# Optimization experiments

Hardware: AMD Instinct MI355X
Metric: run time of the kernel (lower is better)

The kernel has to match this reference:

```python
import jax, jax.numpy as jnp
import numpy as np

M_TOP = 30      # top-M candidates per query
K_NB = 20       # K+1 nearest within candidate set (K=19)
BETA = 0.15


def setup_inputs() -> dict:
    key = jax.random.key(0)
    k1, k2, k3 = jax.random.split(key, 3)
    N, D, B, R = 500000, 512, 4096, 1000
    X = jax.random.normal(k1, (N, D), dtype=jnp.float32)
    Q = jax.random.normal(k2, (B, D), dtype=jnp.float32)
    ranks = jax.random.randint(k3, (R, B), 0, N, dtype=jnp.int64)
    return {"X": X, "Q": Q, "ranks": ranks}


def reference(X, Q, ranks):
    # ranks: [n_ranked, B] -> take top-M candidate ids per query: [B, M]
    rt = ranks.T[:, :M_TOP]                       # [B, M]
    Xt = X[rt]                                    # gather: [B, M, D]
    # batched self-similarity among the M candidates
    sim = jnp.einsum('bmd,bnd->bmn', Xt, Xt)      # [B, M, M]
    # descending sort, keep top K_NB values+indices (== -sort(-sim)[:K], argsort(-sim)[:K])
    vals, idx = jax.lax.top_k(sim, K_NB)          # [B, M, K]
    # weights: first neighbor (self) weight 1.0, rest scaled by beta
    w = jnp.concatenate([jnp.ones_like(vals[..., :1]), vals[..., 1:] * BETA], axis=-1)
    w = w[..., None]                              # [B, M, K, 1]
    # gather neighbor descriptors within each query's candidate set
    # x_g[b,m,k,d] = Xt[b, idx[b,m,k], d]
    x_g = jnp.take_along_axis(Xt[:, None, :, :], idx[..., None], axis=2)  # [B, M, K, D]
    # weighted average over the K neighbors
    x_dba = jnp.sum(x_g * w, axis=2) / jnp.sum(w, axis=2)                 # [B, M, D]
    # rerank candidates against the query descriptor
    scores = jnp.einsum('bd,bmd->bm', Q, x_dba)   # [B, M]
    order = jnp.argsort(-scores, axis=-1)         # [B, M]
    rerank = jnp.take_along_axis(rt, order, axis=1)  # [B, M] final db ids
    return rerank, scores, order, x_dba
```

## Files before the change

### kernel.cpp

```cpp
#include <hip/hip_runtime.h>
#include <stdint.h>

#define MT   30
#define KNB  20
#define DD   512
#define SROW 68
#define MWS  32

#define PR(r) ((((r) & 1) * 15) + ((r) >> 1))

extern "C" __global__ void __launch_bounds__(256, 6)
mdesc_fused(const float* __restrict__ X, const float* __restrict__ Q,
            const int* __restrict__ ranks, float* __restrict__ out, int B)
{
    __shared__ alignas(16) char arrA[MT * SROW * 4];
    __shared__ alignas(16) float QS[DD];
    __shared__ double simS[MT][MT + 1];
    __shared__ double qdotPart[MT][8];
    __shared__ double qdotS[MT];
    __shared__ int    rtS[MT];

    float  (*XtS)[SROW] = (float(*)[SROW])arrA;
    float  (*MwS)[MWS]  = (float(*)[MWS])arrA;
    double *scoreS      = (double*)(arrA + 3840);
    int    *orderS      = (int*)(arrA + 4080);

    const int b = blockIdx.x;
    const int tid = threadIdx.x;

    if (tid < MT) rtS[tid] = ranks[(size_t)tid * B + b];
    __syncthreads();

    const bool isSim = (tid < 120);
    const bool isQ   = (tid >= 128 && tid < 248);
    int i0 = 0, i1 = 0, j0 = 0, j1 = 0;
    if (isSim) {
        int I = 0, rem = tid;
        while (rem >= 15 - I) { rem -= 15 - I; ++I; }
        int J = I + rem;
        i0 = 2 * I; i1 = i0 + 1; j0 = 2 * J; j1 = j0 + 1;
    }
    const int qm = (tid - 128) >> 2;
    const int qs = (tid - 128) & 3;

    double a00 = 0.0, a01 = 0.0, a10 = 0.0, a11 = 0.0;

    for (int st = 0; st < 8; ++st) {
        for (int i = tid; i < MT * 16; i += 256) {
            int row = i >> 4;
            int k = i & 15;
            float4 v = *(const float4*)(X + (size_t)rtS[row] * DD + st * 64 + (k << 2));
            *(float4*)(&XtS[PR(row)][k << 2]) = v;
        }
        if (st == 0 && tid < 128) {
            float4 v = *(const float4*)(Q + (size_t)b * DD + (tid << 2));
            *(float4*)(&QS[tid << 2]) = v;
        }
        __syncthreads();

        if (isSim) {
            const float* R0 = &XtS[PR(i0)][0];
            const float* R1 = &XtS[PR(i1)][0];
            const float* C0 = &XtS[PR(j0)][0];
            const float* C1 = &XtS[PR(j1)][0];
            for (int k = 0; k < 16; ++k) {
                float4 va0 = *(const float4*)(R0 + (k << 2));
                float4 va1 = *(const float4*)(R1 + (k << 2));
                float4 vb0 = *(const float4*)(C0 + (k << 2));
                float4 vb1 = *(const float4*)(C1 + (k << 2));
                const float* A0 = (const float*)&va0;
                const float* A1 = (const float*)&va1;
                const float* B0 = (const float*)&vb0;
                const float* B1 = (const float*)&vb1;
                #pragma unroll
                for (int c = 0; c < 4; ++c) {
                    double x0 = (double)A0[c], x1 = (double)A1[c];
                    double y0 = (double)B0[c], y1 = (double)B1[c];
                    a00 = fma(x0, y0, a00);
                    a01 = fma(x0, y1, a01);
                    a10 = fma(x1, y0, a10);
                    a11 = fma(x1, y1, a11);
                }
            }
            if (st == 3) {
                simS[i0][j0] = a00; simS[i0][j1] = a01;
                simS[i1][j0] = a10; simS[i1][j1] = a11;
                a00 = a01 = a10 = a11 = 0.0;
            }
            if (st == 7) {
                double s00 = simS[i0][j0] + a00;
                double s01 = simS[i0][j1] + a01;
                double s10 = simS[i1][j0] + a10;
                double s11 = simS[i1][j1] + a11;
                simS[i0][j0] = s00; simS[j0][i0] = s00;
                simS[i0][j1] = s01; simS[j1][i0] = s01;
                simS[i1][j0] = s10; simS[j0][i1] = s10;
                simS[i1][j1] = s11; simS[j1][i1] = s11;
            }
        }
        if (isQ && (st & 3) == qs) {
            double acc = 0.0;
            const float* xr = &XtS[PR(qm)][0];
            for (int k = 0; k < 16; ++k) {
                float4 q4 = *(const float4*)(&QS[(st * 16 + k) << 2]);
                float4 x4 = *(const float4*)(xr + (k << 2));
                const float* qq = (const float*)&q4;
                const float* xx = (const float*)&x4;
                #pragma unroll
                for (int c = 0; c < 4; ++c)
                    acc = fma((double)qq[c], (double)xx[c], acc);
            }
            qdotPart[qm][st] = acc;
        }
        __syncthreads();
    }

    for (int i = tid; i < MT * MWS; i += 256) (&MwS[0][0])[i] = 0.0f;
    __syncthreads();

    const size_t sec = (size_t)B * MT;
    if (tid < MT) {
        {
            double acc = 0.0;
            #pragma unroll
            for (int s = 0; s < 8; ++s) acc += qdotPart[tid][s];
            qdotS[tid] = acc;
        }
        const int m = tid;
        unsigned used = 0;
        double Wsum = 0.0, sAcc = 0.0;
        for (int k = 0; k < KNB; ++k) {
            double best = -1.0e300; int bj = 0;
            for (int j = 0; j < MT; ++j) {
                if (used & (1u << j)) continue;
                double v = simS[m][j];
                if (v > best) { best = v; bj = j; }
            }
            used |= (1u << bj);
            double w = (k == 0) ? 1.0 : best * 0.15;
            Wsum += w;
            sAcc = fma(w, qdotS[bj], sAcc);
            MwS[m][bj] = (float)w;
        }
        scoreS[m] = sAcc / Wsum;
        float inv = (float)(1.0 / Wsum);
        for (int j = 0; j < MT; ++j)
            if (used & (1u << j)) MwS[m][j] *= inv;
        double mysc = scoreS[tid];
        int pos = 0;
        for (int j = 0; j < MT; ++j) {
            double v = scoreS[j];
            if (v > mysc || (v == mysc && j < tid)) ++pos;
        }
        orderS[pos] = tid;
        int r = tid;
        int src = orderS[r];
        out[(size_t)b * MT + r]            = (float)rtS[src];
        out[sec + (size_t)b * MT + tid]    = (float)scoreS[tid];
        out[2 * sec + (size_t)b * MT + r]  = (float)src;
    }
    __syncthreads();

    {
        const int sub = tid >> 7;
        const int c   = tid & 127;
        const int r0  = sub * 15;
        float4 acc[15];
        #pragma unroll
        for (int r = 0; r < 15; ++r) acc[r] = make_float4(0.f, 0.f, 0.f, 0.f);

        for (int jg = 0; jg < 15; ++jg) {
            const int ja = 2 * jg, jb = ja + 1;
            float4 xv0 = *(const float4*)(X + (size_t)rtS[ja] * DD + (c << 2));
            float4 xv1 = *(const float4*)(X + (size_t)rtS[jb] * DD + (c << 2));
            #pragma unroll
            for (int r = 0; r < 15; ++r) {
                float2 wv = *(const float2*)&MwS[r0 + r][ja];
                acc[r].x = fmaf(wv.x, xv0.x, acc[r].x);
                acc[r].x = fmaf(wv.y, xv1.x, acc[r].x);
                acc[r].y = fmaf(wv.x, xv0.y, acc[r].y);
                acc[r].y = fmaf(wv.y, xv1.y, acc[r].y);
                acc[r].z = fmaf(wv.x, xv0.z, acc[r].z);
                acc[r].z = fmaf(wv.y, xv1.z, acc[r].z);
                acc[r].w = fmaf(wv.x, xv0.w, acc[r].w);
                acc[r].w = fmaf(wv.y, xv1.w, acc[r].w);
            }
        }

        const size_t xbase = 3 * sec;
        #pragma unroll
        for (int r = 0; r < 15; ++r) {
            *(float4*)(out + xbase + ((size_t)b * MT + (r0 + r)) * DD + (c << 2)) = acc[r];
        }
    }
}

extern "C" void kernel_launch(void* const* d_in, const int* in_sizes, int n_in,
                              void* d_out, int out_size, void* d_ws, size_t ws_size,
                              hipStream_t stream)
{
    const float* X = (const float*)d_in[0];
    const float* Q = (const float*)d_in[1];
    const int* ranks = (const int*)d_in[2];
    const int B = in_sizes[1] / DD;
    mdesc_fused<<<dim3(B), dim3(256), 0, stream>>>(X, Q, ranks, (float*)d_out, B);
}
```

Baseline: 248.6 us.

## Halve block size and use 3x3 register tiles for similarity

Blocks shrink from 256 to 128 threads. The similarity upper triangle is now covered by 55 threads, each computing a 3x3 double tile, instead of 120 threads each doing a 2x2 tile. Each of 30 threads computes its full query dot product, replacing the four-way split. The weighted-average phase loops twice over 15-row groups per thread. This aims to cut idle threads and raise reuse per shared load, but gives less parallelism per block, slower FP64 chains per thread, and drops the padded row permutation that avoided bank conflicts.

```diff
diff --git a/kernel.cpp b/kernel.cpp
--- a/kernel.cpp
+++ b/kernel.cpp
@@ -7,9 +7,7 @@
 #define SROW 68
 #define MWS  32
 
-#define PR(r) ((((r) & 1) * 15) + ((r) >> 1))
-
-extern "C" __global__ void __launch_bounds__(256, 6)
+extern "C" __global__ void __launch_bounds__(128, 4)
 mdesc_fused(const float* __restrict__ X, const float* __restrict__ Q,
             const int* __restrict__ ranks, float* __restrict__ out, int B)
 {
@@ -31,76 +29,89 @@
     if (tid < MT) rtS[tid] = ranks[(size_t)tid * B + b];
     __syncthreads();
 
-    const bool isSim = (tid < 120);
-    const bool isQ   = (tid >= 128 && tid < 248);
-    int i0 = 0, i1 = 0, j0 = 0, j1 = 0;
+    const bool isSim = (tid < 55);
+    int i0 = 0, j0 = 0;
     if (isSim) {
         int I = 0, rem = tid;
-        while (rem >= 15 - I) { rem -= 15 - I; ++I; }
-        int J = I + rem;
-        i0 = 2 * I; i1 = i0 + 1; j0 = 2 * J; j1 = j0 + 1;
-    }
-    const int qm = (tid - 128) >> 2;
-    const int qs = (tid - 128) & 3;
-
-    double a00 = 0.0, a01 = 0.0, a10 = 0.0, a11 = 0.0;
+        while (rem >= 10 - I) { rem -= 10 - I; ++I; }
+        i0 = 3 * I; j0 = 3 * (I + rem);
+    }
+    const bool isQ = (tid >= 64 && tid < 64 + MT);
+    const int qm = tid - 64;
+
+    double a00 = 0.0, a01 = 0.0, a02 = 0.0;
+    double a10 = 0.0, a11 = 0.0, a12 = 0.0;
+    double a20 = 0.0, a21 = 0.0, a22 = 0.0;
 
     for (int st = 0; st < 8; ++st) {
-        for (int i = tid; i < MT * 16; i += 256) {
+        for (int i = tid; i < MT * 16; i += 128) {
             int row = i >> 4;
             int k = i & 15;
             float4 v = *(const float4*)(X + (size_t)rtS[row] * DD + st * 64 + (k << 2));
-            *(float4*)(&XtS[PR(row)][k << 2]) = v;
-        }
-        if (st == 0 && tid < 128) {
+            *(float4*)(&XtS[row][k << 2]) = v;
+        }
+        if (st == 0) {
             float4 v = *(const float4*)(Q + (size_t)b * DD + (tid << 2));
             *(float4*)(&QS[tid << 2]) = v;
         }
         __syncthreads();
 
         if (isSim) {
-            const float* R0 = &XtS[PR(i0)][0];
-            const float* R1 = &XtS[PR(i1)][0];
-            const float* C0 = &XtS[PR(j0)][0];
-            const float* C1 = &XtS[PR(j1)][0];
+            const float* R0 = &XtS[i0][0];
+            const float* R1 = &XtS[i0 + 1][0];
+            const float* R2 = &XtS[i0 + 2][0];
+            const float* C0 = &XtS[j0][0];
+            const float* C1 = &XtS[j0 + 1][0];
+            const float* C2 = &XtS[j0 + 2][0];
             for (int k = 0; k < 16; ++k) {
                 float4 va0 = *(const float4*)(R0 + (k << 2));
                 float4 va1 = *(const float4*)(R1 + (k << 2));
+                float4 va2 = *(const float4*)(R2 + (k << 2));
                 float4 vb0 = *(const float4*)(C0 + (k << 2));
                 float4 vb1 = *(const float4*)(C1 + (k << 2));
+                float4 vb2 = *(const float4*)(C2 + (k << 2));
                 const float* A0 = (const float*)&va0;
                 const float* A1 = (const float*)&va1;
+                const float* A2 = (const float*)&va2;
                 const float* B0 = (const float*)&vb0;
                 const float* B1 = (const float*)&vb1;
+                const float* B2 = (const float*)&vb2;
                 #pragma unroll
                 for (int c = 0; c < 4; ++c) {
-                    double x0 = (double)A0[c], x1 = (double)A1[c];
-                    double y0 = (double)B0[c], y1 = (double)B1[c];
-                    a00 = fma(x0, y0, a00);
-                    a01 = fma(x0, y1, a01);
-                    a10 = fma(x1, y0, a10);
-                    a11 = fma(x1, y1, a11);
+                    double x0 = (double)A0[c], x1 = (double)A1[c], x2 = (double)A2[c];
+                    double y0 = (double)B0[c], y1 = (double)B1[c], y2 = (double)B2[c];
+                    a00 = fma(x0, y0, a00); a01 = fma(x0, y1, a01); a02 = fma(x0, y2, a02);
+                    a10 = fma(x1, y0, a10); a11 = fma(x1, y1, a11); a12 = fma(x1, y2, a12);
+                    a20 = fma(x2, y0, a20); a21 = fma(x2, y1, a21); a22 = fma(x2, y2, a22);
                 }
             }
             if (st == 3) {
-                simS[i0][j0] = a00; simS[i0][j1] = a01;
-                simS[i1][j0] = a10; simS[i1][j1] = a11;
-                a00 = a01 = a10 = a11 = 0.0;
+                simS[i0    ][j0] = a00; simS[i0    ][j0 + 1] = a01; simS[i0    ][j0 + 2] = a02;
+                simS[i0 + 1][j0] = a10; simS[i0 + 1][j0 + 1] = a11; simS[i0 + 1][j0 + 2] = a12;
+                simS[i0 + 2][j0] = a20; simS[i0 + 2][j0 + 1] = a21; simS[i0 + 2][j0 + 2] = a22;
+                a00 = a01 = a02 = a10 = a11 = a12 = a20 = a21 = a22 = 0.0;
             }
             if (st == 7) {
-                double s00 = simS[i0][j0] + a00;
-                double s01 = simS[i0][j1] + a01;
-                double s10 = simS[i1][j0] + a10;
-                double s11 = simS[i1][j1] + a11;
-                simS[i0][j0] = s00; simS[j0][i0] = s00;
-                simS[i0][j1] = s01; simS[j1][i0] = s01;
-                simS[i1][j0] = s10; simS[j0][i1] = s10;
-                simS[i1][j1] = s11; simS[j1][i1] = s11;
-            }
-        }
-        if (isQ && (st & 3) == qs) {
+                double h00v = simS[i0    ][j0]; double h01v = simS[i0    ][j0 + 1]; double h02v = simS[i0    ][j0 + 2];
+                double h10v = simS[i0 + 1][j0]; double h11v = simS[i0 + 1][j0 + 1]; double h12v = simS[i0 + 1][j0 + 2];
+                double h20v = simS[i0 + 2][j0]; double h21v = simS[i0 + 2][j0 + 1]; double h22v = simS[i0 + 2][j0 + 2];
+                double s00 = h00v + a00, s01 = h01v + a01, s02 = h02v + a02;
+                double s10 = h10v + a10, s11 = h11v + a11, s12 = h12v + a12;
+                double s20 = h20v + a20, s21 = h21v + a21, s22 = h22v + a22;
+                simS[i0    ][j0] = s00; simS[j0    ][i0] = s00;
+                simS[i0    ][j0 + 1] = s01; simS[j0 + 1][i0] = s01;
+                simS[i0    ][j0 + 2] = s02; simS[j0 + 2][i0] = s02;
+                simS[i0 + 1][j0] = s10; simS[j0    ][i0 + 1] = s10;
+                simS[i0 + 1][j0 + 1] = s11; simS[j0 + 1][i0 + 1] = s11;
+                simS[i0 + 1][j0 + 2] = s12; simS[j0 + 2][i0 + 1] = s12;
+                simS[i0 + 2][j0] = s20; simS[j0    ][i0 + 2] = s20;
+                simS[i0 + 2][j0 + 1] = s21; simS[j0 + 1][i0 + 2] = s21;
+                simS[i0 + 2][j0 + 2] = s22; simS[j0 + 2][i0 + 2] = s22;
+            }
+        }
+        if (isQ) {
             double acc = 0.0;
-            const float* xr = &XtS[PR(qm)][0];
+            const float* xr = &XtS[qm][0];
             for (int k = 0; k < 16; ++k) {
                 float4 q4 = *(const float4*)(&QS[(st * 16 + k) << 2]);
                 float4 x4 = *(const float4*)(xr + (k << 2));
@@ -115,7 +126,7 @@
         __syncthreads();
     }
 
-    for (int i = tid; i < MT * MWS; i += 256) (&MwS[0][0])[i] = 0.0f;
+    for (int i = tid; i < MT * MWS; i += 128) (&MwS[0][0])[i] = 0.0f;
     __syncthreads();
 
     const size_t sec = (size_t)B * MT;
@@ -162,35 +173,36 @@
     __syncthreads();
 
     {
-        const int sub = tid >> 7;
-        const int c   = tid & 127;
-        const int r0  = sub * 15;
-        float4 acc[15];
+        const int c = tid;
+        const size_t xbase = 3 * sec;
         #pragma unroll
-        for (int r = 0; r < 15; ++r) acc[r] = make_float4(0.f, 0.f, 0.f, 0.f);
-
-        for (int jg = 0; jg < 15; ++jg) {
-            const int ja = 2 * jg, jb = ja + 1;
-            float4 xv0 = *(const float4*)(X + (size_t)rtS[ja] * DD + (c << 2));
-            float4 xv1 = *(const float4*)(X + (size_t)rtS[jb] * DD + (c << 2));
+        for (int g = 0; g < 2; ++g) {
+            const int r0 = g * 15;
+            float4 acc[15];
+            #pragma unroll
+            for (int r = 0; r < 15; ++r) acc[r] = make_float4(0.f, 0.f, 0.f, 0.f);
+
+            for (int jg = 0; jg < 15; ++jg) {
+                const int ja = 2 * jg, jb = ja + 1;
+                float4 xv0 = *(const float4*)(X + (size_t)rtS[ja] * DD + (c << 2));
+                float4 xv1 = *(const float4*)(X + (size_t)rtS[jb] * DD + (c << 2));
+                #pragma unroll
+                for (int r = 0; r < 15; ++r) {
+                    float2 wv = *(const float2*)&MwS[r0 + r][ja];
+                    acc[r].x = fmaf(wv.x, xv0.x, acc[r].x);
+                    acc[r].x = fmaf(wv.y, xv1.x, acc[r].x);
+                    acc[r].y = fmaf(wv.x, xv0.y, acc[r].y);
+                    acc[r].y = fmaf(wv.y, xv1.y, acc[r].y);
+                    acc[r].z = fmaf(wv.x, xv0.z, acc[r].z);
+                    acc[r].z = fmaf(wv.y, xv1.z, acc[r].z);
+                    acc[r].w = fmaf(wv.x, xv0.w, acc[r].w);
+                    acc[r].w = fmaf(wv.y, xv1.w, acc[r].w);
+                }
+            }
             #pragma unroll
             for (int r = 0; r < 15; ++r) {
-                float2 wv = *(const float2*)&MwS[r0 + r][ja];
-                acc[r].x = fmaf(wv.x, xv0.x, acc[r].x);
-                acc[r].x = fmaf(wv.y, xv1.x, acc[r].x);
-                acc[r].y = fmaf(wv.x, xv0.y, acc[r].y);
-                acc[r].y = fmaf(wv.y, xv1.y, acc[r].y);
-                acc[r].z = fmaf(wv.x, xv0.z, acc[r].z);
-                acc[r].z = fmaf(wv.y, xv1.z, acc[r].z);
-                acc[r].w = fmaf(wv.x, xv0.w, acc[r].w);
-                acc[r].w = fmaf(wv.y, xv1.w, acc[r].w);
-            }
-        }
-
-        const size_t xbase = 3 * sec;
-        #pragma unroll
-        for (int r = 0; r < 15; ++r) {
-            *(float4*)(out + xbase + ((size_t)b * MT + (r0 + r)) * DD + (c << 2)) = acc[r];
+                *(float4*)(out + xbase + ((size_t)b * MT + (r0 + r)) * DD + (c << 2)) = acc[r];
+            }
         }
     }
 }
@@ -203,5 +215,5 @@
     const float* Q = (const float*)d_in[1];
     const int* ranks = (const int*)d_in[2];
     const int B = in_sizes[1] / DD;
-    mdesc_fused<<<dim3(B), dim3(256), 0, stream>>>(X, Q, ranks, (float*)d_out, B);
+    mdesc_fused<<<dim3(B), dim3(128), 0, stream>>>(X, Q, ranks, (float*)d_out, B);
 }
```

Result: slower. 289.0 us (+16.3%).
